# Optimization experiments

Hardware: AMD Instinct MI355X
Metric: run time of the kernel (lower is better)

Reference implementation:

```python
import jax, jax.numpy as jnp
import numpy as np

TAU = 1.2  # relaxed-categorical temperature (forward default)


def setup_inputs() -> dict:
    key = jax.random.key(0)
    ks = jax.random.split(key, 8)
    B, F, V, E, H, T = 1024, 2048, 4096, 256, 1024, 32
    n = lambda k, shape: jax.random.normal(k, shape, jnp.float32) * 0.1
    return {
        "t": jax.random.normal(ks[0], (B, F), jnp.float32),
        "embedding": n(ks[1], (V, E)),
        "aff_w": n(ks[2], (H, F)),
        "aff_b": jnp.zeros((H,), jnp.float32),
        "w_ih": n(ks[3], (4 * H, E)),
        "w_hh": n(ks[4], (4 * H, H)),
        "b_ih": jnp.zeros((4 * H,), jnp.float32),
        # PyTorch init: forget-gate bias (second quarter) set to 1
        "b_hh": jnp.zeros((4 * H,), jnp.float32).at[H:2 * H].set(1.0),
        "lp_w": n(ks[5], (V, H)),
        "lp_b": jnp.zeros((V,), jnp.float32),
        "start_token_idx": 1,
        "max_sentence_length": T,
    }


def reference(t, embedding, aff_w, aff_b, w_ih, w_hh, b_ih, b_hh, lp_w, lp_b,
              start_token_idx, max_sentence_length):
    B = t.shape[0]
    H = aff_w.shape[0]
    V = embedding.shape[0]

    h0 = t @ aff_w.T + aff_b                      # [B, H]
    c0 = jnp.zeros((B, H), t.dtype)
    tok0 = jax.nn.one_hot(jnp.full((B,), start_token_idx), V, dtype=t.dtype)

    # Gumbel noise for RelaxedOneHotCategorical rsample, one slab per step
    gumbel = jax.random.gumbel(jax.random.key(42), (max_sentence_length, B, V), t.dtype)

    def step(carry, g):
        h, c, tok = carry
        emb = tok @ embedding                     # [B, E] (one-hot/relaxed matmul)
        gates = emb @ w_ih.T + b_ih + h @ w_hh.T + b_hh  # [B, 4H]
        i, f, gg, o = jnp.split(gates, 4, axis=-1)        # PyTorch gate order i,f,g,o
        c = jax.nn.sigmoid(f) * c + jax.nn.sigmoid(i) * jnp.tanh(gg)
        h = jax.nn.sigmoid(o) * jnp.tanh(c)
        # softmax probs -> relaxed sample: softmax((log p + G)/tau)
        logp = jax.nn.log_softmax(h @ lp_w.T + lp_b, axis=-1)  # [B, V]
        y = jax.nn.softmax((logp + g) / TAU, axis=-1)
        hard = jax.nn.one_hot(jnp.argmax(y, axis=-1), V, dtype=y.dtype)
        tok = jax.lax.stop_gradient(hard - y) + y  # straight-through
        return (h, c, tok), tok

    _, toks = jax.lax.scan(step, (h0, c0, tok0), gumbel)  # toks: [T, B, V]
    message = jnp.concatenate([tok0[None], toks], axis=0)  # [T+1, B, V]
    return jnp.transpose(message, (1, 0, 2))               # [B, T+1, V]
```

## Files before the change

kernel.cpp:

```cpp
#include <hip/hip_runtime.h>
#include <math.h>


typedef _Float16 f16;
typedef f16 f16x8 __attribute__((ext_vector_type(8)));
typedef float f32x4 __attribute__((ext_vector_type(4)));

#define F16_MIN_NORM 6.104e-5f

__device__ __forceinline__ void split_f16(float v, f16& h, f16& l) {
  f16 h0 = (fabsf(v) < F16_MIN_NORM) ? (f16)0.0f : (f16)v;
  float r = (v - (float)h0) * 4096.0f;
  h = h0; l = (f16)r;
}

__device__ __forceinline__ float sigm(float x) { return 1.0f / (1.0f + expf(-x)); }

#define GLOAD_LDS16(gsrc, ldst)                                               \
  __builtin_amdgcn_global_load_lds(                                           \
      (const __attribute__((address_space(1))) unsigned int*)(const void*)(gsrc), \
      (__attribute__((address_space(3))) unsigned int*)(void*)(ldst), 16, 0, 0)


__device__ __forceinline__ unsigned tf_rotl(unsigned x, int r) {
  return (x << r) | (x >> (32 - r));
}

__device__ inline float gumbel_at(unsigned idx) {
  const unsigned ks0 = 0u;
  const unsigned ks1 = 42u;
  const unsigned ks2 = 0x1BD11BDAu ^ ks0 ^ ks1;
  unsigned x0 = 0u + ks0;
  unsigned x1 = idx + ks1;
#define TFR(rot) { x0 += x1; x1 = tf_rotl(x1, rot); x1 ^= x0; }
  TFR(13) TFR(15) TFR(26) TFR(6)
  x0 += ks1; x1 += ks2 + 1u;
  TFR(17) TFR(29) TFR(16) TFR(24)
  x0 += ks2; x1 += ks0 + 2u;
  TFR(13) TFR(15) TFR(26) TFR(6)
  x0 += ks0; x1 += ks1 + 3u;
  TFR(17) TFR(29) TFR(16) TFR(24)
  x0 += ks1; x1 += ks2 + 4u;
  TFR(13) TFR(15) TFR(26) TFR(6)
  x0 += ks2; x1 += ks0 + 5u;
#undef TFR
  const unsigned bits = x0 ^ x1;
  const float f = __uint_as_float((bits >> 9) | 0x3F800000u) - 1.0f;
  const float tiny = 1.17549435082228751e-38f;
  const float u = fmaxf(tiny, f * (1.0f - tiny) + tiny);
  return -logf(-logf(u));
}


__global__ void init_kernel(float* __restrict__ out, const int* __restrict__ startp,
                            int* __restrict__ tok, int Tp1, int V) {
  const int b = blockIdx.x;
  const int start = *startp;
  if (threadIdx.x == 0) tok[b] = start;
  float* orow = out + (size_t)b * Tp1 * V;
  const int tq = start >> 2;
  for (int v4 = threadIdx.x; v4 < V / 4; v4 += blockDim.x) {
    float4 v = make_float4(0.f, 0.f, 0.f, 0.f);
    if (v4 == tq) ((float*)&v)[start & 3] = 1.0f;
    ((float4*)orow)[v4] = v;
  }
}

__global__ void pack_gates_kernel(const float* __restrict__ wih,
                                  const float* __restrict__ whh,
                                  f16* __restrict__ w0, f16* __restrict__ w1,
                                  int E, int H, int K) {
  const int k = blockIdx.x * blockDim.x + threadIdx.x;
  const int p = blockIdx.y;
  if (k >= K) return;
  const int n = ((p >> 4) & 3) * H + ((p >> 6) << 4) + (p & 15);
  const float v = (k < E) ? wih[(size_t)n * E + k] : whh[(size_t)n * H + (k - E)];
  f16 h, l; split_f16(v, h, l);
  w0[(size_t)p * K + k] = h;
  w1[(size_t)p * K + k] = l;
}

__global__ void pack_bias_kernel(const float* __restrict__ bih,
                                 const float* __restrict__ bhh,
                                 float* __restrict__ bi, float* __restrict__ bh, int H) {
  const int p = blockIdx.x * blockDim.x + threadIdx.x;
  const int n = ((p >> 4) & 3) * H + ((p >> 6) << 4) + (p & 15);
  bi[p] = bih[n];
  bh[p] = bhh[n];
}

__global__ void split_kernel(const float* __restrict__ in,
                             f16* __restrict__ o0, f16* __restrict__ o1, int n) {
  const int i = blockIdx.x * blockDim.x + threadIdx.x;
  if (i < n) { f16 h, l; split_f16(in[i], h, l); o0[i] = h; o1[i] = l; }
}


__device__ __forceinline__ void stage_chunk(
    int chunk, int srow, int scol,
    const f16* __restrict__ a0s, const f16* __restrict__ a1s, int lda, int ka, int bm,
    const f16* __restrict__ b0s, const f16* __restrict__ b1s, int ldb, int kb, int bn,
    f16 (*ldsA0)[32], f16 (*ldsA1)[32], f16 (*ldsB0)[32], f16 (*ldsB1)[32])
{
  if (chunk < 8) {
    GLOAD_LDS16(a0s + (size_t)(bm + chunk * 16 + srow) * lda + ka + scol,
                &ldsA0[chunk * 16][0]);
  } else if (chunk < 16) {
    const int s = chunk - 8;
    GLOAD_LDS16(a1s + (size_t)(bm + s * 16 + srow) * lda + ka + scol,
                &ldsA1[s * 16][0]);
  } else if (chunk < 20) {
    const int s = chunk - 16;
    GLOAD_LDS16(b0s + (size_t)(bn + s * 16 + srow) * ldb + kb + scol,
                &ldsB0[s * 16][0]);
  } else {
    const int s = chunk - 20;
    GLOAD_LDS16(b1s + (size_t)(bn + s * 16 + srow) * ldb + kb + scol,
                &ldsB1[s * 16][0]);
  }
}

#define MFMA_DECLS                                                            \
  const int tid  = threadIdx.x;                                               \
  const int lane = tid & 63;                                                  \
  const int wid  = tid >> 6;                                                  \
  const int bm   = blockIdx.y * 128;                                          \
  const int bn   = blockIdx.x * 64;                                           \
  const int wm   = wid * 32;                                                  \
  const int fr   = lane & 15;                                                 \
  const int fk   = (((lane >> 4) ^ ((lane >> 1) & 3)) * 8);                   \
  const int srow = lane >> 2;                                                 \
  const int scol = (((lane & 3) ^ ((lane >> 3) & 3)) * 8);                    \
  f32x4 acc0[2][4], acc1[2][4];                                               \
  _Pragma("unroll") for (int i = 0; i < 2; ++i)                               \
  _Pragma("unroll") for (int j = 0; j < 4; ++j) {                             \
    acc0[i][j] = (f32x4)0.0f; acc1[i][j] = (f32x4)0.0f; }

#define MFMA_LDS_DECL                                                         \
  __shared__ f16 ldsA0[3][128][32], ldsA1[3][128][32],                        \
                 ldsB0[3][64][32],  ldsB1[3][64][32];

#define MFMA_STAGE_TO(buf, a0s, a1s, lda, ka, b0s, b1s, ldb, kb)              \
  { _Pragma("unroll") for (int c = 0; c < 6; ++c)                             \
      stage_chunk(wid * 6 + c, srow, scol, (a0s), (a1s), (lda), (ka), bm,     \
                  (b0s), (b1s), (ldb), (kb), bn,                              \
                  ldsA0[(buf)], ldsA1[(buf)], ldsB0[(buf)], ldsB1[(buf)]); }

#define MFMA_COMPUTE_FROM(buf)                                                \
  {                                                                           \
    f16x8 a0[2], a1[2], b0[4], b1[4];                                         \
    _Pragma("unroll") for (int i = 0; i < 2; ++i) {                           \
      a0[i] = *(const f16x8*)&ldsA0[(buf)][wm + i * 16 + fr][fk];             \
      a1[i] = *(const f16x8*)&ldsA1[(buf)][wm + i * 16 + fr][fk];             \
    }                                                                         \
    _Pragma("unroll") for (int j = 0; j < 4; ++j) {                           \
      b0[j] = *(const f16x8*)&ldsB0[(buf)][j * 16 + fr][fk];                  \
      b1[j] = *(const f16x8*)&ldsB1[(buf)][j * 16 + fr][fk];                  \
    }                                                                         \
    _Pragma("unroll") for (int i = 0; i < 2; ++i)                             \
    _Pragma("unroll") for (int j = 0; j < 4; ++j) {                           \
      acc0[i][j] = __builtin_amdgcn_mfma_f32_16x16x32_f16(a0[i], b0[j], acc0[i][j], 0, 0, 0); \
      acc1[i][j] = __builtin_amdgcn_mfma_f32_16x16x32_f16(a0[i], b1[j], acc1[i][j], 0, 0, 0); \
      acc1[i][j] = __builtin_amdgcn_mfma_f32_16x16x32_f16(a1[i], b0[j], acc1[i][j], 0, 0, 0); \
    }                                                                         \
  }

#define PIPE(NT)                                                              \
  STAGE_T(0, 0)                                                               \
  STAGE_T(1, 1)                                                               \
  for (int t = 0; t < (NT); ++t) {                                            \
    asm volatile("" ::: "memory");                                            \
    if (t + 2 < (NT)) { STAGE_T(((t + 2) % 3), (t + 2)) }                     \
    const int rem = (NT) - 1 - t;                                             \
    if (rem >= 2)      asm volatile("s_waitcnt vmcnt(12)" ::: "memory");      \
    else if (rem == 1) asm volatile("s_waitcnt vmcnt(6)" ::: "memory");       \
    else               asm volatile("s_waitcnt vmcnt(0)" ::: "memory");       \
    __builtin_amdgcn_s_barrier();                                             \
    asm volatile("" ::: "memory");                                            \
    __builtin_amdgcn_s_setprio(1);                                            \
    MFMA_COMPUTE_FROM((t % 3))                                                \
    __builtin_amdgcn_s_setprio(0);                                            \
    asm volatile("" ::: "memory");                                            \
    __builtin_amdgcn_s_barrier();                                             \
  }

__global__ __launch_bounds__(256, 2) void h0_kernel(
    const f16* __restrict__ t0, const f16* __restrict__ t1, int F,
    const f16* __restrict__ aw0, const f16* __restrict__ aw1,
    const float* __restrict__ affb,
    f16* __restrict__ h0p, f16* __restrict__ h1p, int H,
    float* __restrict__ czero)
{
  MFMA_LDS_DECL
  MFMA_DECLS
  const int NT = F / 32;
#define STAGE_T(buf, t) MFMA_STAGE_TO(buf, t0, t1, F, (t) * 32, aw0, aw1, F, (t) * 32)
  PIPE(NT)
#undef STAGE_T
  const int q4 = (lane >> 4) * 4;
  const float s12 = 1.0f / 4096.0f;
#pragma unroll
  for (int j = 0; j < 4; ++j) {
    const int col = bn + j * 16 + fr;
    const float bb = affb[col];
#pragma unroll
    for (int i = 0; i < 2; ++i) {
#pragma unroll
      for (int r = 0; r < 4; ++r) {
        const int row = bm + wm + i * 16 + q4 + r;
        const float v = (acc0[i][j][r] + acc1[i][j][r] * s12) + bb;
        f16 hh, hl; split_f16(v, hh, hl);
        const size_t off = (size_t)row * H + col;
        h0p[off] = hh; h1p[off] = hl;
        czero[off] = 0.0f;
      }
    }
  }
}

__global__ __launch_bounds__(256, 2) void gih_kernel(
    const f16* __restrict__ e0, const f16* __restrict__ e1, int E,
    const f16* __restrict__ w0, const f16* __restrict__ w1, int K,
    const float* __restrict__ bi, const float* __restrict__ bh,
    float* __restrict__ gih, int NP)
{
  MFMA_LDS_DECL
  MFMA_DECLS
  const int NT = E / 32;
#define STAGE_T(buf, t) MFMA_STAGE_TO(buf, e0, e1, E, (t) * 32, w0, w1, K, (t) * 32)
  PIPE(NT)
#undef STAGE_T
  const int q4 = (lane >> 4) * 4;
  const float s12 = 1.0f / 4096.0f;
#pragma unroll
  for (int j = 0; j < 4; ++j) {
    const int col = bn + j * 16 + fr;
    const float bb = bi[col] + bh[col];
#pragma unroll
    for (int i = 0; i < 2; ++i)
#pragma unroll
      for (int r = 0; r < 4; ++r) {
        const int row = bm + wm + i * 16 + q4 + r;
        gih[(size_t)row * NP + col] = (acc0[i][j][r] + acc1[i][j][r] * s12) + bb;
      }
  }
}

__global__ __launch_bounds__(256, 2) void gates_kernel(
    const f16* __restrict__ hin0, const f16* __restrict__ hin1, int H,
    const f16* __restrict__ w0, const f16* __restrict__ w1, int K, int E,
    const float* __restrict__ gih, int NP, const int* __restrict__ tok,
    float* __restrict__ cbuf,
    f16* __restrict__ hout0, f16* __restrict__ hout1)
{
  MFMA_LDS_DECL
  MFMA_DECLS
  const int NT = H / 32;
#define STAGE_T(buf, t) MFMA_STAGE_TO(buf, hin0, hin1, H, (t) * 32, w0, w1, K, E + (t) * 32)
  PIPE(NT)
#undef STAGE_T
  const int q4 = (lane >> 4) * 4;
  const float s12 = 1.0f / 4096.0f;
  const int nunit = (bn >> 2) + fr;
#pragma unroll
  for (int i = 0; i < 2; ++i) {
#pragma unroll
    for (int r = 0; r < 4; ++r) {
      const int row = bm + wm + i * 16 + q4 + r;
      const float* gr = gih + (size_t)tok[row] * NP + bn + fr;
      float gv[4];
#pragma unroll
      for (int j = 0; j < 4; ++j)
        gv[j] = (acc0[i][j][r] + acc1[i][j][r] * s12) + gr[j * 16];
      const size_t off = (size_t)row * H + nunit;
      const float c = cbuf[off];
      const float cn = __fadd_rn(__fmul_rn(sigm(gv[1]), c),
                                 __fmul_rn(sigm(gv[0]), tanhf(gv[2])));
      const float hn = __fmul_rn(sigm(gv[3]), tanhf(cn));
      cbuf[off] = cn;
      f16 hh, hl; split_f16(hn, hh, hl);
      hout0[off] = hh; hout1[off] = hl;
    }
  }
}

__global__ __launch_bounds__(256, 2) void logits_kernel(
    const f16* __restrict__ h0p, const f16* __restrict__ h1p, int H,
    const f16* __restrict__ w0, const f16* __restrict__ w1,
    const float* __restrict__ lpb,
    float* __restrict__ partM, int* __restrict__ partI,
    int step, int B, int V)
{
  MFMA_LDS_DECL
  MFMA_DECLS
  const int NT = H / 32;
#define STAGE_T(buf, t) MFMA_STAGE_TO(buf, h0p, h1p, H, (t) * 32, w0, w1, H, (t) * 32)
  PIPE(NT)
#undef STAGE_T
  const int q4 = (lane >> 4) * 4;
  const float s12 = 1.0f / 4096.0f;
  float bv[4];
#pragma unroll
  for (int j = 0; j < 4; ++j) bv[j] = lpb[bn + j * 16 + fr];
#pragma unroll
  for (int i = 0; i < 2; ++i)
#pragma unroll
    for (int j = 0; j < 4; ++j) {
      const int col = bn + j * 16 + fr;
#pragma unroll
      for (int r = 0; r < 4; ++r) {
        const int row = bm + wm + i * 16 + q4 + r;
        const float logit = (acc0[i][j][r] + acc1[i][j][r] * s12) + bv[j];
        const unsigned gidx = ((unsigned)(step * B + row)) * (unsigned)V + (unsigned)col;
        acc0[i][j][r] = logit + gumbel_at(gidx);
      }
    }
  const int grp = bn >> 6;
#pragma unroll
  for (int i = 0; i < 2; ++i) {
#pragma unroll
    for (int r = 0; r < 4; ++r) {
      float mx = -INFINITY; int ix = 0;
#pragma unroll
      for (int j = 0; j < 4; ++j) {
        const float w = acc0[i][j][r];
        const int col = bn + j * 16 + fr;
        if (w > mx) { mx = w; ix = col; }
      }
#pragma unroll
      for (int m = 1; m < 16; m <<= 1) {
        const float om = __shfl_xor(mx, m, 64);
        const int oi = __shfl_xor(ix, m, 64);
        if (om > mx || (om == mx && oi < ix)) { mx = om; ix = oi; }
      }
      if (fr == 0) {
        const int row = bm + wm + i * 16 + q4 + r;
        partM[(size_t)row * 64 + grp] = mx;
        partI[(size_t)row * 64 + grp] = ix;
      }
    }
  }
}

__global__ __launch_bounds__(256) void finalize_kernel(
    const float* __restrict__ partM, const int* __restrict__ partI,
    float* __restrict__ out, int* __restrict__ tok,
    int step, int Tp1, int V)
{
  const int b = blockIdx.x;
  const int tid = threadIdx.x;
  __shared__ int s_tok;

  if (tid < 64) {
    float mx = partM[(size_t)b * 64 + tid];
    int ix = partI[(size_t)b * 64 + tid];
#pragma unroll
    for (int m = 1; m < 64; m <<= 1) {
      const float om = __shfl_xor(mx, m, 64);
      const int oi = __shfl_xor(ix, m, 64);
      if (om > mx || (om == mx && oi < ix)) { mx = om; ix = oi; }
    }
    if (tid == 0) { s_tok = ix; tok[b] = ix; }
  }
  __syncthreads();
  const int tk = s_tok;

  float* orow = out + ((size_t)b * Tp1 + step + 1) * V;
  const int tq = tk >> 2;
#pragma unroll
  for (int j = 0; j < 4; ++j) {
    const int idx = tid + 256 * j;
    float4 v = make_float4(0.f, 0.f, 0.f, 0.f);
    if (idx == tq) ((float*)&v)[tk & 3] = 1.0f;
    ((float4*)orow)[idx] = v;
  }
}


extern "C" void kernel_launch(void* const* d_in, const int* in_sizes, int n_in,
                              void* d_out, int out_size, void* d_ws, size_t ws_size,
                              hipStream_t stream) {
  const float* t     = (const float*)d_in[0];
  const float* emb   = (const float*)d_in[1];
  const float* affw  = (const float*)d_in[2];
  const float* affb  = (const float*)d_in[3];
  const float* wih   = (const float*)d_in[4];
  const float* whh   = (const float*)d_in[5];
  const float* bih   = (const float*)d_in[6];
  const float* bhh   = (const float*)d_in[7];
  const float* lpw   = (const float*)d_in[8];
  const float* lpb   = (const float*)d_in[9];
  const int*   start = (const int*)d_in[10];
  float* out = (float*)d_out;

  const int H = in_sizes[3];
  const int V = in_sizes[9];
  const int E = in_sizes[1] / V;
  const int F = in_sizes[2] / H;
  const int B = in_sizes[0] / F;
  const int Tp1 = out_size / (B * V);
  const int T = Tp1 - 1;
  const int KG = E + H;
  const int NP = 4 * H;

  char* p = (char*)d_ws;
  float* gihb  = (float*)p; p += (size_t)V * NP * 4;
  float* cbuf  = (float*)p; p += (size_t)B * H * 4;
  f16* hA0[2]; f16* hA1[2];
  hA0[0] = (f16*)p; p += (size_t)B * H * 2;
  hA1[0] = (f16*)p; p += (size_t)B * H * 2;
  hA0[1] = (f16*)p; p += (size_t)B * H * 2;
  hA1[1] = (f16*)p; p += (size_t)B * H * 2;
  f16* wg0 = (f16*)p; p += (size_t)V * KG * 2;
  f16* wg1 = (f16*)p; p += (size_t)V * KG * 2;
  f16* wl0 = (f16*)p; p += (size_t)V * H * 2;
  f16* wl1 = (f16*)p; p += (size_t)V * H * 2;
  f16* t0  = (f16*)p; p += (size_t)B * F * 2;
  f16* t1  = (f16*)p; p += (size_t)B * F * 2;
  f16* aw0 = (f16*)p; p += (size_t)H * F * 2;
  f16* aw1 = (f16*)p; p += (size_t)H * F * 2;
  f16* em0 = (f16*)p; p += (size_t)V * E * 2;
  f16* em1 = (f16*)p; p += (size_t)V * E * 2;
  float* bgi = (float*)p; p += (size_t)NP * 4;
  float* bgh = (float*)p; p += (size_t)NP * 4;
  float* partM = (float*)p; p += (size_t)B * 64 * 4;
  int*   partI = (int*)p;   p += (size_t)B * 64 * 4;
  int*   tokb  = (int*)p;   p += (size_t)B * 4;
  (void)ws_size; (void)n_in;

  init_kernel<<<B, 256, 0, stream>>>(out, start, tokb, Tp1, V);
  pack_gates_kernel<<<dim3((KG + 255) / 256, NP), 256, 0, stream>>>(
      wih, whh, wg0, wg1, E, H, KG);
  pack_bias_kernel<<<NP / 256, 256, 0, stream>>>(bih, bhh, bgi, bgh, H);
  split_kernel<<<(V * H + 255) / 256, 256, 0, stream>>>(lpw, wl0, wl1, V * H);
  split_kernel<<<(B * F + 255) / 256, 256, 0, stream>>>(t, t0, t1, B * F);
  split_kernel<<<(H * F + 255) / 256, 256, 0, stream>>>(affw, aw0, aw1, H * F);
  split_kernel<<<(V * E + 255) / 256, 256, 0, stream>>>(emb, em0, em1, V * E);
  h0_kernel<<<dim3(H / 64, B / 128), 256, 0, stream>>>(
      t0, t1, F, aw0, aw1, affb, hA0[0], hA1[0], H, cbuf);
  gih_kernel<<<dim3(NP / 64, V / 128), 256, 0, stream>>>(
      em0, em1, E, wg0, wg1, KG, bgi, bgh, gihb, NP);

  for (int s = 0; s < T; ++s) {
    const int cur = s & 1, nxt = (s + 1) & 1;
    gates_kernel<<<dim3(NP / 64, B / 128), 256, 0, stream>>>(
        hA0[cur], hA1[cur], H, wg0, wg1, KG, E, gihb, NP, tokb,
        cbuf, hA0[nxt], hA1[nxt]);
    logits_kernel<<<dim3(V / 64, B / 128), 256, 0, stream>>>(
        hA0[nxt], hA1[nxt], H, wl0, wl1, lpb,
        partM, partI, s, B, V);
    finalize_kernel<<<B, 256, 0, stream>>>(
        partM, partI, out, tokb, s, Tp1, V);
  }
}
```

Before: 3.968 ms.

## Enlarge MFMA block tile to 128x128 with 8 waves and 4-stage pipeline

Doubles the N dimension of each workgroup's tile from 64 to 128 by using 8 waves (4 along M, 2 along N), so each staged A tile is reused across twice as many columns. The LDS ring buffer grows from 3 to 4 stages with prefetch depth 3 and adjusted vmcnt waits. This halves the grid size and cuts redundant A-tile global traffic, at the cost of a larger LDS footprint (128 KB per block) that can limit occupancy and fewer blocks to fill the GPU.

New measurement: 3.954 ms. About the same (-0.3%).

```diff
diff --git a/kernel.cpp b/kernel.cpp
--- a/kernel.cpp
+++ b/kernel.cpp
@@ -109,12 +109,12 @@
     const int s = chunk - 8;
     GLOAD_LDS16(a1s + (size_t)(bm + s * 16 + srow) * lda + ka + scol,
                 &ldsA1[s * 16][0]);
-  } else if (chunk < 20) {
+  } else if (chunk < 24) {
     const int s = chunk - 16;
     GLOAD_LDS16(b0s + (size_t)(bn + s * 16 + srow) * ldb + kb + scol,
                 &ldsB0[s * 16][0]);
   } else {
-    const int s = chunk - 20;
+    const int s = chunk - 24;
     GLOAD_LDS16(b1s + (size_t)(bn + s * 16 + srow) * ldb + kb + scol,
                 &ldsB1[s * 16][0]);
   }
@@ -125,8 +125,9 @@
   const int lane = tid & 63;                                                  \
   const int wid  = tid >> 6;                                                  \
   const int bm   = blockIdx.y * 128;                                          \
-  const int bn   = blockIdx.x * 64;                                           \
-  const int wm   = wid * 32;                                                  \
+  const int bn   = blockIdx.x * 128;                                          \
+  const int wm   = (wid & 3) * 32;                                            \
+  const int wn   = (wid >> 2) * 64;                                           \
   const int fr   = lane & 15;                                                 \
   const int fk   = (((lane >> 4) ^ ((lane >> 1) & 3)) * 8);                   \
   const int srow = lane >> 2;                                                 \
@@ -137,12 +138,12 @@
     acc0[i][j] = (f32x4)0.0f; acc1[i][j] = (f32x4)0.0f; }
 
 #define MFMA_LDS_DECL                                                         \
-  __shared__ f16 ldsA0[3][128][32], ldsA1[3][128][32],                        \
-                 ldsB0[3][64][32],  ldsB1[3][64][32];
+  __shared__ f16 ldsA0[4][128][32], ldsA1[4][128][32],                        \
+                 ldsB0[4][128][32], ldsB1[4][128][32];
 
 #define MFMA_STAGE_TO(buf, a0s, a1s, lda, ka, b0s, b1s, ldb, kb)              \
-  { _Pragma("unroll") for (int c = 0; c < 6; ++c)                             \
-      stage_chunk(wid * 6 + c, srow, scol, (a0s), (a1s), (lda), (ka), bm,     \
+  { _Pragma("unroll") for (int c = 0; c < 4; ++c)                             \
+      stage_chunk(wid * 4 + c, srow, scol, (a0s), (a1s), (lda), (ka), bm,     \
                   (b0s), (b1s), (ldb), (kb), bn,                              \
                   ldsA0[(buf)], ldsA1[(buf)], ldsB0[(buf)], ldsB1[(buf)]); }
 
@@ -154,8 +155,8 @@
       a1[i] = *(const f16x8*)&ldsA1[(buf)][wm + i * 16 + fr][fk];             \
     }                                                                         \
     _Pragma("unroll") for (int j = 0; j < 4; ++j) {                           \
-      b0[j] = *(const f16x8*)&ldsB0[(buf)][j * 16 + fr][fk];                  \
-      b1[j] = *(const f16x8*)&ldsB1[(buf)][j * 16 + fr][fk];                  \
+      b0[j] = *(const f16x8*)&ldsB0[(buf)][wn + j * 16 + fr][fk];             \
+      b1[j] = *(const f16x8*)&ldsB1[(buf)][wn + j * 16 + fr][fk];             \
     }                                                                         \
     _Pragma("unroll") for (int i = 0; i < 2; ++i)                             \
     _Pragma("unroll") for (int j = 0; j < 4; ++j) {                           \
@@ -168,23 +169,25 @@
 #define PIPE(NT)                                                              \
   STAGE_T(0, 0)                                                               \
   STAGE_T(1, 1)                                                               \
+  STAGE_T(2, 2)                                                               \
   for (int t = 0; t < (NT); ++t) {                                            \
     asm volatile("" ::: "memory");                                            \
-    if (t + 2 < (NT)) { STAGE_T(((t + 2) % 3), (t + 2)) }                     \
+    if (t + 3 < (NT)) { STAGE_T(((t + 3) & 3), (t + 3)) }                     \
     const int rem = (NT) - 1 - t;                                             \
-    if (rem >= 2)      asm volatile("s_waitcnt vmcnt(12)" ::: "memory");      \
-    else if (rem == 1) asm volatile("s_waitcnt vmcnt(6)" ::: "memory");       \
+    if (rem >= 3)      asm volatile("s_waitcnt vmcnt(12)" ::: "memory");      \
+    else if (rem == 2) asm volatile("s_waitcnt vmcnt(8)" ::: "memory");       \
+    else if (rem == 1) asm volatile("s_waitcnt vmcnt(4)" ::: "memory");       \
     else               asm volatile("s_waitcnt vmcnt(0)" ::: "memory");       \
     __builtin_amdgcn_s_barrier();                                             \
     asm volatile("" ::: "memory");                                            \
     __builtin_amdgcn_s_setprio(1);                                            \
-    MFMA_COMPUTE_FROM((t % 3))                                                \
+    MFMA_COMPUTE_FROM((t & 3))                                                \
     __builtin_amdgcn_s_setprio(0);                                            \
     asm volatile("" ::: "memory");                                            \
     __builtin_amdgcn_s_barrier();                                             \
   }
 
-__global__ __launch_bounds__(256, 2) void h0_kernel(
+__global__ __launch_bounds__(512, 2) void h0_kernel(
     const f16* __restrict__ t0, const f16* __restrict__ t1, int F,
     const f16* __restrict__ aw0, const f16* __restrict__ aw1,
     const float* __restrict__ affb,
@@ -199,9 +202,10 @@
 #undef STAGE_T
   const int q4 = (lane >> 4) * 4;
   const float s12 = 1.0f / 4096.0f;
+  const int cn0 = bn + wn;
 #pragma unroll
   for (int j = 0; j < 4; ++j) {
-    const int col = bn + j * 16 + fr;
+    const int col = cn0 + j * 16 + fr;
     const float bb = affb[col];
 #pragma unroll
     for (int i = 0; i < 2; ++i) {
@@ -218,7 +222,7 @@
   }
 }
 
-__global__ __launch_bounds__(256, 2) void gih_kernel(
+__global__ __launch_bounds__(512, 2) void gih_kernel(
     const f16* __restrict__ e0, const f16* __restrict__ e1, int E,
     const f16* __restrict__ w0, const f16* __restrict__ w1, int K,
     const float* __restrict__ bi, const float* __restrict__ bh,
@@ -232,9 +236,10 @@
 #undef STAGE_T
   const int q4 = (lane >> 4) * 4;
   const float s12 = 1.0f / 4096.0f;
+  const int cn0 = bn + wn;
 #pragma unroll
   for (int j = 0; j < 4; ++j) {
-    const int col = bn + j * 16 + fr;
+    const int col = cn0 + j * 16 + fr;
     const float bb = bi[col] + bh[col];
 #pragma unroll
     for (int i = 0; i < 2; ++i)
@@ -246,7 +251,7 @@
   }
 }
 
-__global__ __launch_bounds__(256, 2) void gates_kernel(
+__global__ __launch_bounds__(512, 2) void gates_kernel(
     const f16* __restrict__ hin0, const f16* __restrict__ hin1, int H,
     const f16* __restrict__ w0, const f16* __restrict__ w1, int K, int E,
     const float* __restrict__ gih, int NP, const int* __restrict__ tok,
@@ -261,13 +266,14 @@
 #undef STAGE_T
   const int q4 = (lane >> 4) * 4;
   const float s12 = 1.0f / 4096.0f;
-  const int nunit = (bn >> 2) + fr;
+  const int cn0 = bn + wn;
+  const int nunit = (cn0 >> 2) + fr;
 #pragma unroll
   for (int i = 0; i < 2; ++i) {
 #pragma unroll
     for (int r = 0; r < 4; ++r) {
       const int row = bm + wm + i * 16 + q4 + r;
-      const float* gr = gih + (size_t)tok[row] * NP + bn + fr;
+      const float* gr = gih + (size_t)tok[row] * NP + cn0 + fr;
       float gv[4];
 #pragma unroll
       for (int j = 0; j < 4; ++j)
@@ -284,7 +290,7 @@
   }
 }
 
-__global__ __launch_bounds__(256, 2) void logits_kernel(
+__global__ __launch_bounds__(512, 2) void logits_kernel(
     const f16* __restrict__ h0p, const f16* __restrict__ h1p, int H,
     const f16* __restrict__ w0, const f16* __restrict__ w1,
     const float* __restrict__ lpb,
@@ -299,14 +305,15 @@
 #undef STAGE_T
   const int q4 = (lane >> 4) * 4;
   const float s12 = 1.0f / 4096.0f;
+  const int cn0 = bn + wn;
   float bv[4];
 #pragma unroll
-  for (int j = 0; j < 4; ++j) bv[j] = lpb[bn + j * 16 + fr];
+  for (int j = 0; j < 4; ++j) bv[j] = lpb[cn0 + j * 16 + fr];
 #pragma unroll
   for (int i = 0; i < 2; ++i)
 #pragma unroll
     for (int j = 0; j < 4; ++j) {
-      const int col = bn + j * 16 + fr;
+      const int col = cn0 + j * 16 + fr;
 #pragma unroll
       for (int r = 0; r < 4; ++r) {
         const int row = bm + wm + i * 16 + q4 + r;
@@ -315,7 +322,7 @@
         acc0[i][j][r] = logit + gumbel_at(gidx);
       }
     }
-  const int grp = bn >> 6;
+  const int grp = cn0 >> 6;
 #pragma unroll
   for (int i = 0; i < 2; ++i) {
 #pragma unroll
@@ -324,7 +331,7 @@
 #pragma unroll
       for (int j = 0; j < 4; ++j) {
         const float w = acc0[i][j][r];
-        const int col = bn + j * 16 + fr;
+        const int col = cn0 + j * 16 + fr;
         if (w > mx) { mx = w; ix = col; }
       }
 #pragma unroll
@@ -436,17 +443,17 @@
   split_kernel<<<(B * F + 255) / 256, 256, 0, stream>>>(t, t0, t1, B * F);
   split_kernel<<<(H * F + 255) / 256, 256, 0, stream>>>(affw, aw0, aw1, H * F);
   split_kernel<<<(V * E + 255) / 256, 256, 0, stream>>>(emb, em0, em1, V * E);
-  h0_kernel<<<dim3(H / 64, B / 128), 256, 0, stream>>>(
+  h0_kernel<<<dim3(H / 128, B / 128), 512, 0, stream>>>(
       t0, t1, F, aw0, aw1, affb, hA0[0], hA1[0], H, cbuf);
-  gih_kernel<<<dim3(NP / 64, V / 128), 256, 0, stream>>>(
+  gih_kernel<<<dim3(NP / 128, V / 128), 512, 0, stream>>>(
       em0, em1, E, wg0, wg1, KG, bgi, bgh, gihb, NP);
 
   for (int s = 0; s < T; ++s) {
     const int cur = s & 1, nxt = (s + 1) & 1;
-    gates_kernel<<<dim3(NP / 64, B / 128), 256, 0, stream>>>(
+    gates_kernel<<<dim3(NP / 128, B / 128), 512, 0, stream>>>(
         hA0[cur], hA1[cur], H, wg0, wg1, KG, E, gihb, NP, tokb,
         cbuf, hA0[nxt], hA1[nxt]);
-    logits_kernel<<<dim3(V / 64, B / 128), 256, 0, stream>>>(
+    logits_kernel<<<dim3(V / 128, B / 128), 512, 0, stream>>>(
         hA0[nxt], hA1[nxt], H, wl0, wl1, lpb,
         partM, partI, s, B, V);
     finalize_kernel<<<B, 256, 0, stream>>>(
```

## Use 8 waves per GEMM block and restructure the LDS pipeline with one barrier

Applied to the files above, without the earlier changes.

All MFMA GEMM kernels now launch 512 threads, each wave owning a 16-row slice instead of 32, so staging work per wave halves. The K-loop is rewritten as a manually unrolled 3-buffer pipeline (2-buffer for h0) with one barrier per iteration and constant vmcnt waits. The aim is more waves in flight to hide latency and less barrier and branch overhead per tile. In exchange, each wave gets less B-operand reuse per LDS read, and the vmcnt counts must match the new per-wave load count.

After: 4.580 ms. 15.4% more time.

```diff
diff --git a/kernel.cpp b/kernel.cpp
--- a/kernel.cpp
+++ b/kernel.cpp
@@ -126,65 +126,73 @@
   const int wid  = tid >> 6;                                                  \
   const int bm   = blockIdx.y * 128;                                          \
   const int bn   = blockIdx.x * 64;                                           \
-  const int wm   = wid * 32;                                                  \
+  const int wm   = wid * 16;                                                  \
   const int fr   = lane & 15;                                                 \
   const int fk   = (((lane >> 4) ^ ((lane >> 1) & 3)) * 8);                   \
   const int srow = lane >> 2;                                                 \
   const int scol = (((lane & 3) ^ ((lane >> 3) & 3)) * 8);                    \
-  f32x4 acc0[2][4], acc1[2][4];                                               \
-  _Pragma("unroll") for (int i = 0; i < 2; ++i)                               \
+  f32x4 acc0[4], acc1[4];                                                     \
   _Pragma("unroll") for (int j = 0; j < 4; ++j) {                             \
-    acc0[i][j] = (f32x4)0.0f; acc1[i][j] = (f32x4)0.0f; }
+    acc0[j] = (f32x4)0.0f; acc1[j] = (f32x4)0.0f; }
 
 #define MFMA_LDS_DECL                                                         \
   __shared__ f16 ldsA0[3][128][32], ldsA1[3][128][32],                        \
                  ldsB0[3][64][32],  ldsB1[3][64][32];
 
 #define MFMA_STAGE_TO(buf, a0s, a1s, lda, ka, b0s, b1s, ldb, kb)              \
-  { _Pragma("unroll") for (int c = 0; c < 6; ++c)                             \
-      stage_chunk(wid * 6 + c, srow, scol, (a0s), (a1s), (lda), (ka), bm,     \
+  { _Pragma("unroll") for (int c = 0; c < 3; ++c)                             \
+      stage_chunk(wid * 3 + c, srow, scol, (a0s), (a1s), (lda), (ka), bm,     \
                   (b0s), (b1s), (ldb), (kb), bn,                              \
                   ldsA0[(buf)], ldsA1[(buf)], ldsB0[(buf)], ldsB1[(buf)]); }
 
 #define MFMA_COMPUTE_FROM(buf)                                                \
   {                                                                           \
-    f16x8 a0[2], a1[2], b0[4], b1[4];                                         \
-    _Pragma("unroll") for (int i = 0; i < 2; ++i) {                           \
-      a0[i] = *(const f16x8*)&ldsA0[(buf)][wm + i * 16 + fr][fk];             \
-      a1[i] = *(const f16x8*)&ldsA1[(buf)][wm + i * 16 + fr][fk];             \
-    }                                                                         \
+    f16x8 a0, a1, b0[4], b1[4];                                               \
+    a0 = *(const f16x8*)&ldsA0[(buf)][wm + fr][fk];                           \
+    a1 = *(const f16x8*)&ldsA1[(buf)][wm + fr][fk];                           \
     _Pragma("unroll") for (int j = 0; j < 4; ++j) {                           \
       b0[j] = *(const f16x8*)&ldsB0[(buf)][j * 16 + fr][fk];                  \
       b1[j] = *(const f16x8*)&ldsB1[(buf)][j * 16 + fr][fk];                  \
     }                                                                         \
-    _Pragma("unroll") for (int i = 0; i < 2; ++i)                             \
     _Pragma("unroll") for (int j = 0; j < 4; ++j) {                           \
-      acc0[i][j] = __builtin_amdgcn_mfma_f32_16x16x32_f16(a0[i], b0[j], acc0[i][j], 0, 0, 0); \
-      acc1[i][j] = __builtin_amdgcn_mfma_f32_16x16x32_f16(a0[i], b1[j], acc1[i][j], 0, 0, 0); \
-      acc1[i][j] = __builtin_amdgcn_mfma_f32_16x16x32_f16(a1[i], b0[j], acc1[i][j], 0, 0, 0); \
+      acc0[j] = __builtin_amdgcn_mfma_f32_16x16x32_f16(a0, b0[j], acc0[j], 0, 0, 0); \
+      acc1[j] = __builtin_amdgcn_mfma_f32_16x16x32_f16(a0, b1[j], acc1[j], 0, 0, 0); \
+      acc1[j] = __builtin_amdgcn_mfma_f32_16x16x32_f16(a1, b0[j], acc1[j], 0, 0, 0); \
     }                                                                         \
   }
 
-#define PIPE(NT)                                                              \
+#define PIPE_ITER(buf, DOSTAGE, VM)                                           \
+  asm volatile("s_waitcnt vmcnt(" #VM ")" ::: "memory");                      \
+  __builtin_amdgcn_s_barrier();                                               \
+  asm volatile("" ::: "memory");                                              \
+  DOSTAGE                                                                     \
+  asm volatile("" ::: "memory");                                              \
+  __builtin_amdgcn_s_setprio(1);                                              \
+  MFMA_COMPUTE_FROM(buf)                                                      \
+  __builtin_amdgcn_s_setprio(0);                                              \
+  asm volatile("" ::: "memory");
+
+#define PIPE3(NT)                                                             \
+  STAGE_T(0, 0) STAGE_T(1, 1)                                                 \
+  {                                                                           \
+    int tt = 0;                                                               \
+    for (; tt + 4 < (NT); tt += 3) {                                          \
+      PIPE_ITER(0, STAGE_T(2, tt + 2), 3)                                     \
+      PIPE_ITER(1, STAGE_T(0, tt + 3), 3)                                     \
+      PIPE_ITER(2, STAGE_T(1, tt + 4), 3)                                     \
+    }                                                                         \
+    PIPE_ITER(0, {}, 3)                                                       \
+    PIPE_ITER(1, {}, 0)                                                       \
+  }
+
+#define PIPE2(NT)                                                             \
   STAGE_T(0, 0)                                                               \
-  STAGE_T(1, 1)                                                               \
-  for (int t = 0; t < (NT); ++t) {                                            \
-    asm volatile("" ::: "memory");                                            \
-    if (t + 2 < (NT)) { STAGE_T(((t + 2) % 3), (t + 2)) }                     \
-    const int rem = (NT) - 1 - t;                                             \
-    if (rem >= 2)      asm volatile("s_waitcnt vmcnt(12)" ::: "memory");      \
-    else if (rem == 1) asm volatile("s_waitcnt vmcnt(6)" ::: "memory");       \
-    else               asm volatile("s_waitcnt vmcnt(0)" ::: "memory");       \
-    __builtin_amdgcn_s_barrier();                                             \
-    asm volatile("" ::: "memory");                                            \
-    __builtin_amdgcn_s_setprio(1);                                            \
-    MFMA_COMPUTE_FROM((t % 3))                                                \
-    __builtin_amdgcn_s_setprio(0);                                            \
-    asm volatile("" ::: "memory");                                            \
-    __builtin_amdgcn_s_barrier();                                             \
-  }
-
-__global__ __launch_bounds__(256, 2) void h0_kernel(
+  for (int tt = 0; tt < (NT); tt += 2) {                                      \
+    PIPE_ITER(0, if (tt + 1 < (NT)) { STAGE_T(1, tt + 1) }, 0)                \
+    PIPE_ITER(1, if (tt + 2 < (NT)) { STAGE_T(0, tt + 2) }, 0)                \
+  }
+
+__global__ __launch_bounds__(512, 4) void h0_kernel(
     const f16* __restrict__ t0, const f16* __restrict__ t1, int F,
     const f16* __restrict__ aw0, const f16* __restrict__ aw1,
     const float* __restrict__ affb,
@@ -195,7 +203,7 @@
   MFMA_DECLS
   const int NT = F / 32;
 #define STAGE_T(buf, t) MFMA_STAGE_TO(buf, t0, t1, F, (t) * 32, aw0, aw1, F, (t) * 32)
-  PIPE(NT)
+  PIPE2(NT)
 #undef STAGE_T
   const int q4 = (lane >> 4) * 4;
   const float s12 = 1.0f / 4096.0f;
@@ -204,21 +212,18 @@
     const int col = bn + j * 16 + fr;
     const float bb = affb[col];
 #pragma unroll
-    for (int i = 0; i < 2; ++i) {
-#pragma unroll
-      for (int r = 0; r < 4; ++r) {
-        const int row = bm + wm + i * 16 + q4 + r;
-        const float v = (acc0[i][j][r] + acc1[i][j][r] * s12) + bb;
-        f16 hh, hl; split_f16(v, hh, hl);
-        const size_t off = (size_t)row * H + col;
-        h0p[off] = hh; h1p[off] = hl;
-        czero[off] = 0.0f;
-      }
-    }
-  }
-}
-
-__global__ __launch_bounds__(256, 2) void gih_kernel(
+    for (int r = 0; r < 4; ++r) {
+      const int row = bm + wm + q4 + r;
+      const float v = (acc0[j][r] + acc1[j][r] * s12) + bb;
+      f16 hh, hl; split_f16(v, hh, hl);
+      const size_t off = (size_t)row * H + col;
+      h0p[off] = hh; h1p[off] = hl;
+      czero[off] = 0.0f;
+    }
+  }
+}
+
+__global__ __launch_bounds__(512, 4) void gih_kernel(
     const f16* __restrict__ e0, const f16* __restrict__ e1, int E,
     const f16* __restrict__ w0, const f16* __restrict__ w1, int K,
     const float* __restrict__ bi, const float* __restrict__ bh,
@@ -228,7 +233,7 @@
   MFMA_DECLS
   const int NT = E / 32;
 #define STAGE_T(buf, t) MFMA_STAGE_TO(buf, e0, e1, E, (t) * 32, w0, w1, K, (t) * 32)
-  PIPE(NT)
+  PIPE3(NT)
 #undef STAGE_T
   const int q4 = (lane >> 4) * 4;
   const float s12 = 1.0f / 4096.0f;
@@ -237,16 +242,14 @@
     const int col = bn + j * 16 + fr;
     const float bb = bi[col] + bh[col];
 #pragma unroll
-    for (int i = 0; i < 2; ++i)
-#pragma unroll
-      for (int r = 0; r < 4; ++r) {
-        const int row = bm + wm + i * 16 + q4 + r;
-        gih[(size_t)row * NP + col] = (acc0[i][j][r] + acc1[i][j][r] * s12) + bb;
-      }
-  }
-}
-
-__global__ __launch_bounds__(256, 2) void gates_kernel(
+    for (int r = 0; r < 4; ++r) {
+      const int row = bm + wm + q4 + r;
+      gih[(size_t)row * NP + col] = (acc0[j][r] + acc1[j][r] * s12) + bb;
+    }
+  }
+}
+
+__global__ __launch_bounds__(512, 4) void gates_kernel(
     const f16* __restrict__ hin0, const f16* __restrict__ hin1, int H,
     const f16* __restrict__ w0, const f16* __restrict__ w1, int K, int E,
     const float* __restrict__ gih, int NP, const int* __restrict__ tok,
@@ -257,34 +260,31 @@
   MFMA_DECLS
   const int NT = H / 32;
 #define STAGE_T(buf, t) MFMA_STAGE_TO(buf, hin0, hin1, H, (t) * 32, w0, w1, K, E + (t) * 32)
-  PIPE(NT)
+  PIPE3(NT)
 #undef STAGE_T
   const int q4 = (lane >> 4) * 4;
   const float s12 = 1.0f / 4096.0f;
   const int nunit = (bn >> 2) + fr;
 #pragma unroll
-  for (int i = 0; i < 2; ++i) {
-#pragma unroll
-    for (int r = 0; r < 4; ++r) {
-      const int row = bm + wm + i * 16 + q4 + r;
-      const float* gr = gih + (size_t)tok[row] * NP + bn + fr;
-      float gv[4];
-#pragma unroll
-      for (int j = 0; j < 4; ++j)
-        gv[j] = (acc0[i][j][r] + acc1[i][j][r] * s12) + gr[j * 16];
-      const size_t off = (size_t)row * H + nunit;
-      const float c = cbuf[off];
-      const float cn = __fadd_rn(__fmul_rn(sigm(gv[1]), c),
-                                 __fmul_rn(sigm(gv[0]), tanhf(gv[2])));
-      const float hn = __fmul_rn(sigm(gv[3]), tanhf(cn));
-      cbuf[off] = cn;
-      f16 hh, hl; split_f16(hn, hh, hl);
-      hout0[off] = hh; hout1[off] = hl;
-    }
-  }
-}
-
-__global__ __launch_bounds__(256, 2) void logits_kernel(
+  for (int r = 0; r < 4; ++r) {
+    const int row = bm + wm + q4 + r;
+    const float* gr = gih + (size_t)tok[row] * NP + bn + fr;
+    float gv[4];
+#pragma unroll
+    for (int j = 0; j < 4; ++j)
+      gv[j] = (acc0[j][r] + acc1[j][r] * s12) + gr[j * 16];
+    const size_t off = (size_t)row * H + nunit;
+    const float c = cbuf[off];
+    const float cn = __fadd_rn(__fmul_rn(sigm(gv[1]), c),
+                               __fmul_rn(sigm(gv[0]), tanhf(gv[2])));
+    const float hn = __fmul_rn(sigm(gv[3]), tanhf(cn));
+    cbuf[off] = cn;
+    f16 hh, hl; split_f16(hn, hh, hl);
+    hout0[off] = hh; hout1[off] = hl;
+  }
+}
+
+__global__ __launch_bounds__(512, 4) void logits_kernel(
     const f16* __restrict__ h0p, const f16* __restrict__ h1p, int H,
     const f16* __restrict__ w0, const f16* __restrict__ w1,
     const float* __restrict__ lpb,
@@ -295,7 +295,7 @@
   MFMA_DECLS
   const int NT = H / 32;
 #define STAGE_T(buf, t) MFMA_STAGE_TO(buf, h0p, h1p, H, (t) * 32, w0, w1, H, (t) * 32)
-  PIPE(NT)
+  PIPE3(NT)
 #undef STAGE_T
   const int q4 = (lane >> 4) * 4;
   const float s12 = 1.0f / 4096.0f;
@@ -303,41 +303,36 @@
 #pragma unroll
   for (int j = 0; j < 4; ++j) bv[j] = lpb[bn + j * 16 + fr];
 #pragma unroll
-  for (int i = 0; i < 2; ++i)
+  for (int j = 0; j < 4; ++j) {
+    const int col = bn + j * 16 + fr;
+#pragma unroll
+    for (int r = 0; r < 4; ++r) {
+      const int row = bm + wm + q4 + r;
+      const float logit = (acc0[j][r] + acc1[j][r] * s12) + bv[j];
+      const unsigned gidx = ((unsigned)(step * B + row)) * (unsigned)V + (unsigned)col;
+      acc0[j][r] = logit + gumbel_at(gidx);
+    }
+  }
+  const int grp = bn >> 6;
+#pragma unroll
+  for (int r = 0; r < 4; ++r) {
+    float mx = -INFINITY; int ix = 0;
 #pragma unroll
     for (int j = 0; j < 4; ++j) {
+      const float w = acc0[j][r];
       const int col = bn + j * 16 + fr;
-#pragma unroll
-      for (int r = 0; r < 4; ++r) {
-        const int row = bm + wm + i * 16 + q4 + r;
-        const float logit = (acc0[i][j][r] + acc1[i][j][r] * s12) + bv[j];
-        const unsigned gidx = ((unsigned)(step * B + row)) * (unsigned)V + (unsigned)col;
-        acc0[i][j][r] = logit + gumbel_at(gidx);
-      }
-    }
-  const int grp = bn >> 6;
-#pragma unroll
-  for (int i = 0; i < 2; ++i) {
-#pragma unroll
-    for (int r = 0; r < 4; ++r) {
-      float mx = -INFINITY; int ix = 0;
-#pragma unroll
-      for (int j = 0; j < 4; ++j) {
-        const float w = acc0[i][j][r];
-        const int col = bn + j * 16 + fr;
-        if (w > mx) { mx = w; ix = col; }
-      }
-#pragma unroll
-      for (int m = 1; m < 16; m <<= 1) {
-        const float om = __shfl_xor(mx, m, 64);
-        const int oi = __shfl_xor(ix, m, 64);
-        if (om > mx || (om == mx && oi < ix)) { mx = om; ix = oi; }
-      }
-      if (fr == 0) {
-        const int row = bm + wm + i * 16 + q4 + r;
-        partM[(size_t)row * 64 + grp] = mx;
-        partI[(size_t)row * 64 + grp] = ix;
-      }
+      if (w > mx) { mx = w; ix = col; }
+    }
+#pragma unroll
+    for (int m = 1; m < 16; m <<= 1) {
+      const float om = __shfl_xor(mx, m, 64);
+      const int oi = __shfl_xor(ix, m, 64);
+      if (om > mx || (om == mx && oi < ix)) { mx = om; ix = oi; }
+    }
+    if (fr == 0) {
+      const int row = bm + wm + q4 + r;
+      partM[(size_t)row * 64 + grp] = mx;
+      partI[(size_t)row * 64 + grp] = ix;
     }
   }
 }
@@ -436,17 +431,17 @@
   split_kernel<<<(B * F + 255) / 256, 256, 0, stream>>>(t, t0, t1, B * F);
   split_kernel<<<(H * F + 255) / 256, 256, 0, stream>>>(affw, aw0, aw1, H * F);
   split_kernel<<<(V * E + 255) / 256, 256, 0, stream>>>(emb, em0, em1, V * E);
-  h0_kernel<<<dim3(H / 64, B / 128), 256, 0, stream>>>(
+  h0_kernel<<<dim3(H / 64, B / 128), 512, 0, stream>>>(
       t0, t1, F, aw0, aw1, affb, hA0[0], hA1[0], H, cbuf);
-  gih_kernel<<<dim3(NP / 64, V / 128), 256, 0, stream>>>(
+  gih_kernel<<<dim3(NP / 64, V / 128), 512, 0, stream>>>(
       em0, em1, E, wg0, wg1, KG, bgi, bgh, gihb, NP);
 
   for (int s = 0; s < T; ++s) {
     const int cur = s & 1, nxt = (s + 1) & 1;
-    gates_kernel<<<dim3(NP / 64, B / 128), 256, 0, stream>>>(
+    gates_kernel<<<dim3(NP / 64, B / 128), 512, 0, stream>>>(
         hA0[cur], hA1[cur], H, wg0, wg1, KG, E, gihb, NP, tokb,
         cbuf, hA0[nxt], hA1[nxt]);
-    logits_kernel<<<dim3(V / 64, B / 128), 256, 0, stream>>>(
+    logits_kernel<<<dim3(V / 64, B / 128), 512, 0, stream>>>(
         hA0[nxt], hA1[nxt], H, wl0, wl1, lpb,
         partM, partI, s, B, V);
     finalize_kernel<<<B, 256, 0, stream>>>(
```
